# Optimization experiments

Measured on AMD Instinct MI355X. Metric: run time of the kernel, lower is better.

## Reference

```python
import jax, jax.numpy as jnp
import numpy as np

B, N, D, P, HMUL, K = 2, 4096, 64, 64, 4, 16
H = D * HMUL  # attn_mlp hidden = 256
EPS = 1e-5


def setup_inputs() -> dict:
    key = jax.random.key(0)
    ks = jax.random.split(key, 18)
    def lin(k, fan_in, shape):
        return (jax.random.normal(k, shape, dtype=jnp.float32) / np.sqrt(fan_in)).astype(jnp.float32)
    return {
        "x": jax.random.normal(ks[0], (B, N, D), dtype=jnp.float32),
        "pos": jax.random.uniform(ks[1], (B, N, 3), dtype=jnp.float32),
        "w_qkv": lin(ks[2], D, (D, 3 * D)), "b_qkv": jnp.zeros((3 * D,), jnp.float32),
        "w_p1": lin(ks[3], 3, (3, P)),     "b_p1": jnp.zeros((P,), jnp.float32),
        "w_p2": lin(ks[4], P, (P, D)),     "b_p2": jnp.zeros((D,), jnp.float32),
        "w_a1": lin(ks[5], D, (D, H)),     "b_a1": jnp.zeros((H,), jnp.float32),
        "w_a2": lin(ks[6], H, (H, D)),     "b_a2": jnp.zeros((D,), jnp.float32),
        "w_fc": lin(ks[7], D, (D, D)),     "b_fc": jnp.zeros((D,), jnp.float32),
        "gamma": jnp.ones((D,), jnp.float32), "beta": jnp.zeros((D,), jnp.float32),
    }


def reference(x, pos, w_qkv, b_qkv, w_p1, b_p1, w_p2, b_p2,
              w_a1, b_a1, w_a2, b_a2, w_fc, b_fc, gamma, beta):
    residual = x
    qkv = x @ w_qkv + b_qkv                      # [B,N,3D]
    q, k, v = jnp.split(qkv, 3, axis=-1)         # each [B,N,D]

    # full O(N^2) pairwise distances for KNN (smallest-k)
    rel = pos[:, :, None, :] - pos[:, None, :, :]       # [B,N,N,3]
    dist = jnp.sqrt(jnp.sum(rel * rel, axis=-1))        # [B,N,N]
    _, idx = jax.lax.top_k(-dist, K)                    # [B,N,K] nearest indices

    # gather neighbors (gather commutes with the pointwise MLPs the torch
    # code applies before its neighbor_select, so math is identical)
    gather = jax.vmap(lambda arr, i: arr[i])            # arr:[N,*], i:[N,K] -> [N,K,*]
    k_nb = gather(k, idx)                               # [B,N,K,D]
    v_nb = gather(v, idx)                               # [B,N,K,D]
    pos_nb = gather(pos, idx)                           # [B,N,K,3]

    qk_map = q[:, :, None, :] - k_nb                    # [B,N,K,D]
    rel_nb = pos[:, :, None, :] - pos_nb                # [B,N,K,3]
    pos_emb = jax.nn.relu(rel_nb @ w_p1 + b_p1) @ w_p2 + b_p2   # [B,N,K,D]

    h = qk_map + pos_emb
    scores = jax.nn.relu(h @ w_a1 + b_a1) @ w_a2 + b_a2          # [B,N,K,D]
    attn = jax.nn.softmax(scores, axis=-2)                       # over K neighbors
    agg = jnp.sum(attn * v_nb, axis=-2)                          # [B,N,D]

    agg = agg @ w_fc + b_fc
    # BatchNorm1d over channel dim D (training-mode batch stats over B and N)
    mean = jnp.mean(agg, axis=(0, 1))
    var = jnp.mean(jnp.square(agg - mean), axis=(0, 1))
    agg = (agg - mean) * jax.lax.rsqrt(var + EPS) * gamma + beta
    return jax.nn.relu(agg) + residual
```

## Files before the change

kernel.cpp:

```cpp
#include <hip/hip_runtime.h>
#include <hip/hip_bf16.h>
#include <math.h>

#define NPTS 4096
#define KNB 16
#define CAP 384
#define QPB 8

typedef __attribute__((ext_vector_type(8))) short bf16x8;
typedef __attribute__((ext_vector_type(4))) float f32x4;
#define MFMA16(a, b, c) __builtin_amdgcn_mfma_f32_16x16x32_bf16(a, b, c, 0, 0, 0)

__device__ __forceinline__ unsigned short f2bf(float f) {
  unsigned int u = __float_as_uint(f);
  unsigned int r = (u + 0x7fffu + ((u >> 16) & 1u)) >> 16;
  return (unsigned short)r;
}

__global__ __launch_bounds__(256) void qkv_pack_kernel(
    const float* __restrict__ x, const float* __restrict__ w_qkv,
    const float* __restrict__ b_qkv, float* __restrict__ qkv,
    const float* __restrict__ w_a1, const float* __restrict__ w_a2,
    const float* __restrict__ w_p2, unsigned short* __restrict__ pk1,
    unsigned short* __restrict__ pk2, unsigned short* __restrict__ pkp,
    float* __restrict__ stats) {
  int tid = threadIdx.x, bid = blockIdx.x;

  if (bid == 272) {
    if (tid < 128) stats[tid] = 0.f;
    return;
  }
  if (bid >= 128) {
    int e = (bid - 128) * 256 + tid;
    if (e < 16384) {
      int j = e & 7, lane = (e >> 3) & 63, t = e >> 9;
      int ks = t & 1, nt = t >> 1;
      int k = ks * 32 + ((lane >> 4) << 3) + j, n = nt * 16 + (lane & 15);
      pk1[e] = f2bf(w_a1[k * 256 + n]);
    } else if (e < 32768) {
      int e2 = e - 16384;
      int j = e2 & 7, lane = (e2 >> 3) & 63, t = e2 >> 9;
      int ks = t & 7, nt = t >> 3;
      int k = ks * 32 + ((lane >> 4) << 3) + j, n = nt * 16 + (lane & 15);
      pk2[e2] = f2bf(w_a2[k * 64 + n]);
    } else if (e < 36864) {
      int e3 = e - 32768;
      int j = e3 & 7, lane = (e3 >> 3) & 63, t = e3 >> 9;
      int ks = t & 1, nt = t >> 1;
      int k = ks * 32 + ((lane >> 4) << 3) + j, n = nt * 16 + (lane & 15);
      pkp[e3] = f2bf(w_p2[k * 64 + n]);
    }
    return;
  }

  int lane = tid & 63, w = tid >> 6;
  int m = lane & 15, quad = lane >> 4;
  int r0w = bid * 64 + w * 16;

  const float* xr = x + (size_t)(r0w + m) * 64;
  float xa[8], xb[8];
  *(float4*)&xa[0] = *(const float4*)(xr + quad * 8);
  *(float4*)&xa[4] = *(const float4*)(xr + quad * 8 + 4);
  *(float4*)&xb[0] = *(const float4*)(xr + 32 + quad * 8);
  *(float4*)&xb[4] = *(const float4*)(xr + 32 + quad * 8 + 4);
  bf16x8 a0, a1;
#pragma unroll
  for (int j = 0; j < 8; ++j) {
    a0[j] = (short)f2bf(xa[j]);
    a1[j] = (short)f2bf(xb[j]);
  }

#pragma unroll 4
  for (int nt = 0; nt < 12; ++nt) {
    int n = nt * 16 + m;
    int k0 = quad * 8;
    bf16x8 b0, b1;
#pragma unroll
    for (int j = 0; j < 8; ++j) {
      b0[j] = (short)f2bf(w_qkv[(size_t)(k0 + j) * 192 + n]);
      b1[j] = (short)f2bf(w_qkv[(size_t)(32 + k0 + j) * 192 + n]);
    }
    f32x4 acc = {0.f, 0.f, 0.f, 0.f};
    acc = MFMA16(a0, b0, acc);
    acc = MFMA16(a1, b1, acc);
    float bb = b_qkv[n];
#pragma unroll
    for (int i = 0; i < 4; ++i)
      qkv[(size_t)(r0w + quad * 4 + i) * 192 + n] = acc[i] + bb;
  }
}

__global__ __launch_bounds__(256, 4) void fused_kernel(
    const float* __restrict__ qkv, const float* __restrict__ pos,
    const unsigned short* __restrict__ pk1,
    const unsigned short* __restrict__ pk2,
    const unsigned short* __restrict__ pkp, const float* __restrict__ w_p1,
    const float* __restrict__ b_p1, const float* __restrict__ b_p2,
    const float* __restrict__ b_a1, const float* __restrict__ b_a2,
    const float* __restrict__ w_fc, const float* __restrict__ b_fc,
    float* __restrict__ y, float* __restrict__ stats) {
  __shared__ __align__(16) char smem[25216];
  __shared__ int s_idx[128];

  int tid = threadIdx.x, lane = tid & 63, w = tid >> 6;
  int m = lane & 15, quad = lane >> 4;
  int g0 = blockIdx.x * QPB;
  int b = g0 >> 12;
  const float* posb = pos + (size_t)b * NPTS * 3;

  {
    unsigned int(*cbits)[CAP] = (unsigned int(*)[CAP])smem;
    int(*cidx)[CAP] = (int(*)[CAP])(smem + 12288);
    unsigned long long* wmin = (unsigned long long*)(smem + 24576);
    float* sretry = (float*)(smem + 24608);
    unsigned int* scnt = (unsigned int*)(smem + 24640);
    unsigned long long* sprev = (unsigned long long*)(smem + 24672);
    int* sany = (int*)(smem + 24680);

    float qx[QPB], qy[QPB], qz[QPB];
#pragma unroll
    for (int q = 0; q < QPB; ++q) {
      int i = (g0 + q) & (NPTS - 1);
      qx[q] = posb[i * 3 + 0];
      qy[q] = posb[i * 3 + 1];
      qz[q] = posb[i * 3 + 2];
    }
    if (tid < QPB) scnt[tid] = 0;
    if (tid == 0) sany[0] = 0;
    __syncthreads();

    const float T2 = 0.015625f;
    for (int c = 0; c < NPTS / 256; ++c) {
      int j = c * 256 + tid;
      int j3 = j * 3;
      float px = posb[j3 + 0], py = posb[j3 + 1], pz = posb[j3 + 2];
#pragma unroll
      for (int q = 0; q < QPB; ++q) {
        float dx = qx[q] - px, dy = qy[q] - py, dz = qz[q] - pz;
        float d2 = fmaf(dz, dz, fmaf(dy, dy, dx * dx));
        bool hit = d2 < T2;
        unsigned long long mask = __ballot(hit);
        if (mask) {
          if (hit) {
            unsigned int p = atomicAdd(&scnt[q], 1u);
            if (p < CAP) {
              cbits[q][p] = __float_as_uint(d2);
              cidx[q][p] = j;
            }
          }
        }
      }
    }
    __syncthreads();

    if (tid < QPB) {
      int q = tid;
      unsigned int n = scnt[q];
      float nt = 0.f;
      if (n < KNB) nt = 0.0625f;
      else if (n > CAP) nt = 0.00390625f;
      sretry[q] = nt;
      if (nt != 0.f) {
        scnt[q] = 0;
        sany[0] = 1;
      }
    }
    __syncthreads();

    if (sany[0]) {
      float tr[QPB];
#pragma unroll
      for (int q = 0; q < QPB; ++q) tr[q] = sretry[q];
      for (int c = 0; c < NPTS / 256; ++c) {
        int j = c * 256 + tid;
        int j3 = j * 3;
        float px = posb[j3 + 0], py = posb[j3 + 1], pz = posb[j3 + 2];
#pragma unroll
        for (int q = 0; q < QPB; ++q) {
          if (tr[q] != 0.f) {
            float dx = qx[q] - px, dy = qy[q] - py, dz = qz[q] - pz;
            float d2 = fmaf(dz, dz, fmaf(dy, dy, dx * dx));
            bool hit = d2 < tr[q];
            unsigned long long mask = __ballot(hit);
            if (mask) {
              if (hit) {
                unsigned int p = atomicAdd(&scnt[q], 1u);
                if (p < CAP) {
                  cbits[q][p] = __float_as_uint(d2);
                  cidx[q][p] = j;
                }
              }
            }
          }
        }
      }
      __syncthreads();
    }

    for (int qq = 0; qq < 2; ++qq) {
      int q = w * 2 + qq;
      int L = (int)scnt[q];
      if (L >= KNB && L <= CAP) {
        for (int i = lane; i < L; i += 64) {
          unsigned long long ki = ((unsigned long long)cbits[q][i] << 32) |
                                  (unsigned int)cidx[q][i];
          int rank = 0;
          for (int mm = 0; mm < L; ++mm) {
            unsigned long long km = ((unsigned long long)cbits[q][mm] << 32) |
                                    (unsigned int)cidx[q][mm];
            rank += km < ki;
          }
          if (rank < KNB) s_idx[q * KNB + rank] = cidx[q][i];
        }
      }
    }
    __syncthreads();

    for (int q = 0; q < QPB; ++q) {
      unsigned int n = scnt[q];
      if (n < KNB || n > CAP) {
        unsigned long long prev = 0ull;
        for (int r = 0; r < KNB; ++r) {
          unsigned long long best = ~0ull;
          for (int c = 0; c < NPTS / 256; ++c) {
            int j = c * 256 + tid;
            float dx = qx[q] - posb[j * 3 + 0];
            float dy = qy[q] - posb[j * 3 + 1];
            float dz = qz[q] - posb[j * 3 + 2];
            float d2 = fmaf(dz, dz, fmaf(dy, dy, dx * dx));
            unsigned long long key =
                ((unsigned long long)__float_as_uint(d2) << 32) |
                (unsigned int)j;
            bool ok = (r == 0) || (key > prev);
            best = (ok && key < best) ? key : best;
          }
#pragma unroll
          for (int off = 32; off > 0; off >>= 1) {
            unsigned long long o = __shfl_down(best, off);
            best = best < o ? best : o;
          }
          if (lane == 0) wmin[w] = best;
          __syncthreads();
          if (tid == 0) {
            unsigned long long m0 = wmin[0], m1 = wmin[1];
            unsigned long long m2 = wmin[2], m3 = wmin[3];
            unsigned long long a = m0 < m1 ? m0 : m1;
            unsigned long long d = m2 < m3 ? m2 : m3;
            a = a < d ? a : d;
            s_idx[q * KNB + r] = (int)(unsigned int)a;
            sprev[0] = a;
          }
          __syncthreads();
          prev = sprev[0];
          __syncthreads();
        }
      }
    }
  }
  __syncthreads();

  unsigned short(*region)[72] = (unsigned short(*)[72])smem;
  float(*s_rel)[32][3] = (float(*)[32][3])(smem + 18432);

  if (lane < 32) {
    int row = 32 * w + lane;
    int p = lane >> 4;
    int g = g0 + 2 * w + p;
    int jb = (b << 12) | s_idx[row];
    s_rel[w][lane][0] = pos[(size_t)g * 3 + 0] - pos[(size_t)jb * 3 + 0];
    s_rel[w][lane][1] = pos[(size_t)g * 3 + 1] - pos[(size_t)jb * 3 + 1];
    s_rel[w][lane][2] = pos[(size_t)g * 3 + 2] - pos[(size_t)jb * 3 + 2];
  }

  {
    float w0 = w_p1[lane], w1 = w_p1[64 + lane], w2 = w_p1[128 + lane];
    float bp = b_p1[lane];
    for (int rl = 0; rl < 32; ++rl) {
      int row = 32 * w + rl;
      float rx = s_rel[w][rl][0], ry = s_rel[w][rl][1], rz = s_rel[w][rl][2];
      float e = fmaf(rz, w2, fmaf(ry, w1, fmaf(rx, w0, bp)));
      region[row][lane] = f2bf(fmaxf(e, 0.f));
    }
  }

  {
    bf16x8 ea0[2], ea1[2];
#pragma unroll
    for (int p = 0; p < 2; ++p) {
      ea0[p] = *(const bf16x8*)&region[32 * w + 16 * p + m][quad * 8];
      ea1[p] = *(const bf16x8*)&region[32 * w + 16 * p + m][32 + quad * 8];
    }
#pragma unroll
    for (int nt = 0; nt < 4; ++nt) {
      bf16x8 b0 = *(const bf16x8*)(pkp + ((size_t)(nt * 2 + 0) * 64 + lane) * 8);
      bf16x8 b1 = *(const bf16x8*)(pkp + ((size_t)(nt * 2 + 1) * 64 + lane) * 8);
      int col = nt * 16 + m;
      float bp2 = b_p2[col];
#pragma unroll
      for (int p = 0; p < 2; ++p) {
        f32x4 acc = {0.f, 0.f, 0.f, 0.f};
        acc = MFMA16(ea0[p], b0, acc);
        acc = MFMA16(ea1[p], b1, acc);
        int g = g0 + 2 * w + p;
        float qv = qkv[(size_t)g * 192 + col];
#pragma unroll
        for (int i = 0; i < 4; ++i) {
          int row = 32 * w + 16 * p + quad * 4 + i;
          int jb = (b << 12) | s_idx[row];
          float kv = qkv[(size_t)jb * 192 + 64 + col];
          region[row][col] = f2bf(qv - kv + acc[i] + bp2);
        }
      }
    }
  }

  float vreg[2][4][4];
#pragma unroll
  for (int p = 0; p < 2; ++p)
#pragma unroll
    for (int i = 0; i < 4; ++i) {
      int row = 32 * w + 16 * p + quad * 4 + i;
      int jb = (b << 12) | s_idx[row];
      const float* vr = qkv + (size_t)jb * 192 + 128;
#pragma unroll
      for (int nt2 = 0; nt2 < 4; ++nt2) vreg[p][nt2][i] = vr[nt2 * 16 + m];
    }

  bf16x8 ha0[2], ha1[2];
#pragma unroll
  for (int p = 0; p < 2; ++p) {
    ha0[p] = *(const bf16x8*)&region[32 * w + 16 * p + m][quad * 8];
    ha1[p] = *(const bf16x8*)&region[32 * w + 16 * p + m][32 + quad * 8];
  }
  f32x4 acc2[2][4];
#pragma unroll
  for (int p = 0; p < 2; ++p)
#pragma unroll
    for (int nt2 = 0; nt2 < 4; ++nt2) acc2[p][nt2] = (f32x4){0.f, 0.f, 0.f, 0.f};

  unsigned short(*s_tc)[72] = (unsigned short(*)[72])(smem + w * 4608);

#pragma unroll
  for (int c = 0; c < 4; ++c) {
#pragma unroll
    for (int ntc = 0; ntc < 4; ++ntc) {
      int nt = 4 * c + ntc;
      bf16x8 b0 = *(const bf16x8*)(pk1 + ((size_t)(nt * 2 + 0) * 64 + lane) * 8);
      bf16x8 b1 = *(const bf16x8*)(pk1 + ((size_t)(nt * 2 + 1) * 64 + lane) * 8);
      int coll = ntc * 16 + m;
      float ba = b_a1[nt * 16 + m];
#pragma unroll
      for (int p = 0; p < 2; ++p) {
        f32x4 t = {0.f, 0.f, 0.f, 0.f};
        t = MFMA16(ha0[p], b0, t);
        t = MFMA16(ha1[p], b1, t);
#pragma unroll
        for (int i = 0; i < 4; ++i)
          s_tc[16 * p + quad * 4 + i][coll] = f2bf(fmaxf(t[i] + ba, 0.f));
      }
    }
#pragma unroll
    for (int sub = 0; sub < 2; ++sub) {
      int ks = c * 2 + sub;
      bf16x8 a[2];
#pragma unroll
      for (int p = 0; p < 2; ++p)
        a[p] = *(const bf16x8*)&s_tc[16 * p + m][sub * 32 + quad * 8];
#pragma unroll
      for (int nt2 = 0; nt2 < 4; ++nt2) {
        bf16x8 bb =
            *(const bf16x8*)(pk2 + ((size_t)(nt2 * 8 + ks) * 64 + lane) * 8);
#pragma unroll
        for (int p = 0; p < 2; ++p) acc2[p][nt2] = MFMA16(a[p], bb, acc2[p][nt2]);
      }
    }
  }

  float ba2[4];
#pragma unroll
  for (int nt2 = 0; nt2 < 4; ++nt2) ba2[nt2] = b_a2[nt2 * 16 + m];
  float aggv[2][4];
#pragma unroll
  for (int p = 0; p < 2; ++p) {
#pragma unroll
    for (int nt2 = 0; nt2 < 4; ++nt2) {
      float sc[4];
#pragma unroll
      for (int i = 0; i < 4; ++i) sc[i] = acc2[p][nt2][i] + ba2[nt2];
      float mx = fmaxf(fmaxf(sc[0], sc[1]), fmaxf(sc[2], sc[3]));
      mx = fmaxf(mx, __shfl_xor(mx, 16));
      mx = fmaxf(mx, __shfl_xor(mx, 32));
      float ex[4], ss = 0.f;
#pragma unroll
      for (int i = 0; i < 4; ++i) {
        ex[i] = exp2f((sc[i] - mx) * 1.4426950408889634f);
        ss += ex[i];
      }
      ss += __shfl_xor(ss, 16);
      ss += __shfl_xor(ss, 32);
      float nu = 0.f;
#pragma unroll
      for (int i = 0; i < 4; ++i) nu = fmaf(ex[i], vreg[p][nt2][i], nu);
      nu += __shfl_xor(nu, 16);
      nu += __shfl_xor(nu, 32);
      aggv[p][nt2] = nu / ss;
    }
  }
  __syncthreads();

  float* s_agg = (float*)smem;
  if (quad == 0) {
#pragma unroll
    for (int p = 0; p < 2; ++p)
#pragma unroll
      for (int nt2 = 0; nt2 < 4; ++nt2)
        s_agg[(2 * w + p) * 64 + nt2 * 16 + m] = aggv[p][nt2];
  }
  __syncthreads();

  {
    int c = lane, r = w;
    float acc0 = b_fc[c], acc1 = b_fc[c];
    for (int d = 0; d < 64; ++d) {
      float wv = w_fc[d * 64 + c];
      acc0 = fmaf(s_agg[r * 64 + d], wv, acc0);
      acc1 = fmaf(s_agg[(r + 4) * 64 + d], wv, acc1);
    }
    y[(size_t)(g0 + r) * 64 + c] = acc0;
    y[(size_t)(g0 + r + 4) * 64 + c] = acc1;
    float* s_red = (float*)(smem + 2048);
    float* s_red2 = (float*)(smem + 3072);
    s_red[w * 64 + c] = acc0 + acc1;
    s_red2[w * 64 + c] = acc0 * acc0 + acc1 * acc1;
  }
  __syncthreads();
  if (tid < 64) {
    float* s_red = (float*)(smem + 2048);
    float* s_red2 = (float*)(smem + 3072);
    float s = s_red[tid] + s_red[64 + tid] + s_red[128 + tid] + s_red[192 + tid];
    float s2 =
        s_red2[tid] + s_red2[64 + tid] + s_red2[128 + tid] + s_red2[192 + tid];
    atomicAdd(&stats[tid], s);
    atomicAdd(&stats[64 + tid], s2);
  }
}

__global__ __launch_bounds__(256) void bn_kernel(
    const float* __restrict__ y, const float* __restrict__ x,
    const float* __restrict__ stats, const float* __restrict__ gamma,
    const float* __restrict__ beta, float* __restrict__ out) {
  size_t o = (size_t)blockIdx.x * 256 + threadIdx.x;
  int c = (int)(o & 63);
  const float inv_n = 1.f / 8192.f;
  float mean = stats[c] * inv_n;
  float var = stats[64 + c] * inv_n - mean * mean;
  float inv = rsqrtf(var + 1e-5f);
  float v = (y[o] - mean) * inv * gamma[c] + beta[c];
  out[o] = fmaxf(v, 0.f) + x[o];
}

extern "C" void kernel_launch(void* const* d_in, const int* in_sizes, int n_in,
                              void* d_out, int out_size, void* d_ws,
                              size_t ws_size, hipStream_t stream) {
  const float* x = (const float*)d_in[0];
  const float* pos = (const float*)d_in[1];
  const float* w_qkv = (const float*)d_in[2];
  const float* b_qkv = (const float*)d_in[3];
  const float* w_p1 = (const float*)d_in[4];
  const float* b_p1 = (const float*)d_in[5];
  const float* w_p2 = (const float*)d_in[6];
  const float* b_p2 = (const float*)d_in[7];
  const float* w_a1 = (const float*)d_in[8];
  const float* b_a1 = (const float*)d_in[9];
  const float* w_a2 = (const float*)d_in[10];
  const float* b_a2 = (const float*)d_in[11];
  const float* w_fc = (const float*)d_in[12];
  const float* b_fc = (const float*)d_in[13];
  const float* gamma = (const float*)d_in[14];
  const float* beta = (const float*)d_in[15];

  char* ws = (char*)d_ws;
  float* qkv = (float*)(ws + 0);
  float* y = (float*)(ws + 8912896);
  float* stats = (float*)(ws + 11010048);
  unsigned short* pk1 = (unsigned short*)(ws + 11010560);
  unsigned short* pk2 = (unsigned short*)(ws + 11043328);
  unsigned short* pkp = (unsigned short*)(ws + 11076096);

  hipLaunchKernelGGL(qkv_pack_kernel, dim3(273), dim3(256), 0, stream, x,
                     w_qkv, b_qkv, qkv, w_a1, w_a2, w_p2, pk1, pk2, pkp,
                     stats);
  hipLaunchKernelGGL(fused_kernel, dim3(1024), dim3(256), 0, stream, qkv, pos,
                     pk1, pk2, pkp, w_p1, b_p1, b_p2, b_a1, b_a2, w_fc, b_fc,
                     y, stats);
  hipLaunchKernelGGL(bn_kernel, dim3(2048), dim3(256), 0, stream, y, x, stats,
                     gamma, beta, (float*)d_out);
}
```

Baseline: 151.9 us.

## Halve queries per block and use a density-adaptive per-query KNN radius

Each block of the fused kernel now handles 4 query points instead of 8. Per-block shared memory drops, the candidate cap is halved, the launch-bounds occupancy hint is raised and the grid is doubled. The fixed KNN search radius is replaced with a per-query radius estimated from uniform point density with boundary clipping, aiming for about 48 candidates, and retry thresholds now scale from that radius. The aim is higher occupancy and fewer retry passes for queries near the box edges. The cost is that every block rescans all 4096 positions for fewer queries, and the radius estimate assumes a roughly uniform point cloud, falling back to retries otherwise.

```diff
diff --git a/kernel.cpp b/kernel.cpp
--- a/kernel.cpp
+++ b/kernel.cpp
@@ -4,8 +4,8 @@
 
 #define NPTS 4096
 #define KNB 16
-#define CAP 384
-#define QPB 8
+#define CAP 192
+#define QPB 4
 
 typedef __attribute__((ext_vector_type(8))) short bf16x8;
 typedef __attribute__((ext_vector_type(4))) float f32x4;
@@ -90,7 +90,7 @@
   }
 }
 
-__global__ __launch_bounds__(256, 4) void fused_kernel(
+__global__ __launch_bounds__(256, 8) void fused_kernel(
     const float* __restrict__ qkv, const float* __restrict__ pos,
     const unsigned short* __restrict__ pk1,
     const unsigned short* __restrict__ pk2,
@@ -99,8 +99,8 @@
     const float* __restrict__ b_a1, const float* __restrict__ b_a2,
     const float* __restrict__ w_fc, const float* __restrict__ b_fc,
     float* __restrict__ y, float* __restrict__ stats) {
-  __shared__ __align__(16) char smem[25216];
-  __shared__ int s_idx[128];
+  __shared__ __align__(16) char smem[9984];
+  __shared__ int s_idx[64];
 
   int tid = threadIdx.x, lane = tid & 63, w = tid >> 6;
   int m = lane & 15, quad = lane >> 4;
@@ -110,14 +110,14 @@
 
   {
     unsigned int(*cbits)[CAP] = (unsigned int(*)[CAP])smem;
-    int(*cidx)[CAP] = (int(*)[CAP])(smem + 12288);
-    unsigned long long* wmin = (unsigned long long*)(smem + 24576);
-    float* sretry = (float*)(smem + 24608);
-    unsigned int* scnt = (unsigned int*)(smem + 24640);
-    unsigned long long* sprev = (unsigned long long*)(smem + 24672);
-    int* sany = (int*)(smem + 24680);
-
-    float qx[QPB], qy[QPB], qz[QPB];
+    int(*cidx)[CAP] = (int(*)[CAP])(smem + 3072);
+    unsigned long long* wmin = (unsigned long long*)(smem + 6144);
+    float* sretry = (float*)(smem + 6176);
+    unsigned int* scnt = (unsigned int*)(smem + 6192);
+    unsigned long long* sprev = (unsigned long long*)(smem + 6208);
+    int* sany = (int*)(smem + 6216);
+
+    float qx[QPB], qy[QPB], qz[QPB], t2q[QPB];
 #pragma unroll
     for (int q = 0; q < QPB; ++q) {
       int i = (g0 + q) & (NPTS - 1);
@@ -125,11 +125,26 @@
       qy[q] = posb[i * 3 + 1];
       qz[q] = posb[i * 3 + 2];
     }
+#pragma unroll
+    for (int q = 0; q < QPB; ++q) {
+      float r = 0.141f;
+#pragma unroll
+      for (int it = 0; it < 3; ++it) {
+        float inv2r = 0.5f / r;
+        float fx = (fminf(qx[q] + r, 1.f) - fmaxf(qx[q] - r, 0.f)) * inv2r;
+        float fy = (fminf(qy[q] + r, 1.f) - fmaxf(qy[q] - r, 0.f)) * inv2r;
+        float fz = (fminf(qz[q] + r, 1.f) - fmaxf(qz[q] - r, 0.f)) * inv2r;
+        float expn = 17157.28f * r * r * r * fx * fy * fz;
+        float s = exp2f(0.33333334f * log2f(48.f / expn));
+        s = fminf(fmaxf(s, 0.7f), 1.6f);
+        r = fminf(r * s, 0.32f);
+      }
+      t2q[q] = r * r;
+    }
     if (tid < QPB) scnt[tid] = 0;
     if (tid == 0) sany[0] = 0;
     __syncthreads();
 
-    const float T2 = 0.015625f;
     for (int c = 0; c < NPTS / 256; ++c) {
       int j = c * 256 + tid;
       int j3 = j * 3;
@@ -138,7 +153,7 @@
       for (int q = 0; q < QPB; ++q) {
         float dx = qx[q] - px, dy = qy[q] - py, dz = qz[q] - pz;
         float d2 = fmaf(dz, dz, fmaf(dy, dy, dx * dx));
-        bool hit = d2 < T2;
+        bool hit = d2 < t2q[q];
         unsigned long long mask = __ballot(hit);
         if (mask) {
           if (hit) {
@@ -157,8 +172,8 @@
       int q = tid;
       unsigned int n = scnt[q];
       float nt = 0.f;
-      if (n < KNB) nt = 0.0625f;
-      else if (n > CAP) nt = 0.00390625f;
+      if (n < KNB) nt = t2q[q] * 4.f;
+      else if (n > CAP) nt = t2q[q] * 0.4f;
       sretry[q] = nt;
       if (nt != 0.f) {
         scnt[q] = 0;
@@ -197,8 +212,8 @@
       __syncthreads();
     }
 
-    for (int qq = 0; qq < 2; ++qq) {
-      int q = w * 2 + qq;
+    {
+      int q = w;
       int L = (int)scnt[q];
       if (L >= KNB && L <= CAP) {
         for (int i = lane; i < L; i += 64) {
@@ -260,12 +275,11 @@
   __syncthreads();
 
   unsigned short(*region)[72] = (unsigned short(*)[72])smem;
-  float(*s_rel)[32][3] = (float(*)[32][3])(smem + 18432);
-
-  if (lane < 32) {
-    int row = 32 * w + lane;
-    int p = lane >> 4;
-    int g = g0 + 2 * w + p;
+  float(*s_rel)[16][3] = (float(*)[16][3])(smem + 9216);
+
+  if (lane < 16) {
+    int row = 16 * w + lane;
+    int g = g0 + w;
     int jb = (b << 12) | s_idx[row];
     s_rel[w][lane][0] = pos[(size_t)g * 3 + 0] - pos[(size_t)jb * 3 + 0];
     s_rel[w][lane][1] = pos[(size_t)g * 3 + 1] - pos[(size_t)jb * 3 + 1];
@@ -275,8 +289,8 @@
   {
     float w0 = w_p1[lane], w1 = w_p1[64 + lane], w2 = w_p1[128 + lane];
     float bp = b_p1[lane];
-    for (int rl = 0; rl < 32; ++rl) {
-      int row = 32 * w + rl;
+    for (int rl = 0; rl < 16; ++rl) {
+      int row = 16 * w + rl;
       float rx = s_rel[w][rl][0], ry = s_rel[w][rl][1], rz = s_rel[w][rl][2];
       float e = fmaf(rz, w2, fmaf(ry, w1, fmaf(rx, w0, bp)));
       region[row][lane] = f2bf(fmaxf(e, 0.f));
@@ -284,61 +298,46 @@
   }
 
   {
-    bf16x8 ea0[2], ea1[2];
-#pragma unroll
-    for (int p = 0; p < 2; ++p) {
-      ea0[p] = *(const bf16x8*)&region[32 * w + 16 * p + m][quad * 8];
-      ea1[p] = *(const bf16x8*)&region[32 * w + 16 * p + m][32 + quad * 8];
-    }
+    bf16x8 ea0 = *(const bf16x8*)&region[16 * w + m][quad * 8];
+    bf16x8 ea1 = *(const bf16x8*)&region[16 * w + m][32 + quad * 8];
+    int g = g0 + w;
 #pragma unroll
     for (int nt = 0; nt < 4; ++nt) {
       bf16x8 b0 = *(const bf16x8*)(pkp + ((size_t)(nt * 2 + 0) * 64 + lane) * 8);
       bf16x8 b1 = *(const bf16x8*)(pkp + ((size_t)(nt * 2 + 1) * 64 + lane) * 8);
       int col = nt * 16 + m;
       float bp2 = b_p2[col];
-#pragma unroll
-      for (int p = 0; p < 2; ++p) {
-        f32x4 acc = {0.f, 0.f, 0.f, 0.f};
-        acc = MFMA16(ea0[p], b0, acc);
-        acc = MFMA16(ea1[p], b1, acc);
-        int g = g0 + 2 * w + p;
-        float qv = qkv[(size_t)g * 192 + col];
-#pragma unroll
-        for (int i = 0; i < 4; ++i) {
-          int row = 32 * w + 16 * p + quad * 4 + i;
-          int jb = (b << 12) | s_idx[row];
-          float kv = qkv[(size_t)jb * 192 + 64 + col];
-          region[row][col] = f2bf(qv - kv + acc[i] + bp2);
-        }
-      }
-    }
-  }
-
-  float vreg[2][4][4];
-#pragma unroll
-  for (int p = 0; p < 2; ++p)
-#pragma unroll
-    for (int i = 0; i < 4; ++i) {
-      int row = 32 * w + 16 * p + quad * 4 + i;
-      int jb = (b << 12) | s_idx[row];
-      const float* vr = qkv + (size_t)jb * 192 + 128;
-#pragma unroll
-      for (int nt2 = 0; nt2 < 4; ++nt2) vreg[p][nt2][i] = vr[nt2 * 16 + m];
-    }
-
-  bf16x8 ha0[2], ha1[2];
-#pragma unroll
-  for (int p = 0; p < 2; ++p) {
-    ha0[p] = *(const bf16x8*)&region[32 * w + 16 * p + m][quad * 8];
-    ha1[p] = *(const bf16x8*)&region[32 * w + 16 * p + m][32 + quad * 8];
-  }
-  f32x4 acc2[2][4];
-#pragma unroll
-  for (int p = 0; p < 2; ++p)
-#pragma unroll
-    for (int nt2 = 0; nt2 < 4; ++nt2) acc2[p][nt2] = (f32x4){0.f, 0.f, 0.f, 0.f};
-
-  unsigned short(*s_tc)[72] = (unsigned short(*)[72])(smem + w * 4608);
+      f32x4 acc = {0.f, 0.f, 0.f, 0.f};
+      acc = MFMA16(ea0, b0, acc);
+      acc = MFMA16(ea1, b1, acc);
+      float qv = qkv[(size_t)g * 192 + col];
+#pragma unroll
+      for (int i = 0; i < 4; ++i) {
+        int row = 16 * w + quad * 4 + i;
+        int jb = (b << 12) | s_idx[row];
+        float kv = qkv[(size_t)jb * 192 + 64 + col];
+        region[row][col] = f2bf(qv - kv + acc[i] + bp2);
+      }
+    }
+  }
+
+  float vreg[4][4];
+#pragma unroll
+  for (int i = 0; i < 4; ++i) {
+    int row = 16 * w + quad * 4 + i;
+    int jb = (b << 12) | s_idx[row];
+    const float* vr = qkv + (size_t)jb * 192 + 128;
+#pragma unroll
+    for (int nt2 = 0; nt2 < 4; ++nt2) vreg[nt2][i] = vr[nt2 * 16 + m];
+  }
+
+  bf16x8 ha0 = *(const bf16x8*)&region[16 * w + m][quad * 8];
+  bf16x8 ha1 = *(const bf16x8*)&region[16 * w + m][32 + quad * 8];
+  f32x4 acc2[4];
+#pragma unroll
+  for (int nt2 = 0; nt2 < 4; ++nt2) acc2[nt2] = (f32x4){0.f, 0.f, 0.f, 0.f};
+
+  unsigned short(*s_tc)[72] = (unsigned short(*)[72])(smem + w * 2304);
 
 #pragma unroll
   for (int c = 0; c < 4; ++c) {
@@ -349,29 +348,22 @@
       bf16x8 b1 = *(const bf16x8*)(pk1 + ((size_t)(nt * 2 + 1) * 64 + lane) * 8);
       int coll = ntc * 16 + m;
       float ba = b_a1[nt * 16 + m];
-#pragma unroll
-      for (int p = 0; p < 2; ++p) {
-        f32x4 t = {0.f, 0.f, 0.f, 0.f};
-        t = MFMA16(ha0[p], b0, t);
-        t = MFMA16(ha1[p], b1, t);
-#pragma unroll
-        for (int i = 0; i < 4; ++i)
-          s_tc[16 * p + quad * 4 + i][coll] = f2bf(fmaxf(t[i] + ba, 0.f));
-      }
+      f32x4 t = {0.f, 0.f, 0.f, 0.f};
+      t = MFMA16(ha0, b0, t);
+      t = MFMA16(ha1, b1, t);
+#pragma unroll
+      for (int i = 0; i < 4; ++i)
+        s_tc[quad * 4 + i][coll] = f2bf(fmaxf(t[i] + ba, 0.f));
     }
 #pragma unroll
     for (int sub = 0; sub < 2; ++sub) {
       int ks = c * 2 + sub;
-      bf16x8 a[2];
-#pragma unroll
-      for (int p = 0; p < 2; ++p)
-        a[p] = *(const bf16x8*)&s_tc[16 * p + m][sub * 32 + quad * 8];
+      bf16x8 a = *(const bf16x8*)&s_tc[m][sub * 32 + quad * 8];
 #pragma unroll
       for (int nt2 = 0; nt2 < 4; ++nt2) {
         bf16x8 bb =
             *(const bf16x8*)(pk2 + ((size_t)(nt2 * 8 + ks) * 64 + lane) * 8);
-#pragma unroll
-        for (int p = 0; p < 2; ++p) acc2[p][nt2] = MFMA16(a[p], bb, acc2[p][nt2]);
+        acc2[nt2] = MFMA16(a, bb, acc2[nt2]);
       }
     }
   }
@@ -379,64 +371,55 @@
   float ba2[4];
 #pragma unroll
   for (int nt2 = 0; nt2 < 4; ++nt2) ba2[nt2] = b_a2[nt2 * 16 + m];
-  float aggv[2][4];
-#pragma unroll
-  for (int p = 0; p < 2; ++p) {
-#pragma unroll
-    for (int nt2 = 0; nt2 < 4; ++nt2) {
-      float sc[4];
-#pragma unroll
-      for (int i = 0; i < 4; ++i) sc[i] = acc2[p][nt2][i] + ba2[nt2];
-      float mx = fmaxf(fmaxf(sc[0], sc[1]), fmaxf(sc[2], sc[3]));
-      mx = fmaxf(mx, __shfl_xor(mx, 16));
-      mx = fmaxf(mx, __shfl_xor(mx, 32));
-      float ex[4], ss = 0.f;
-#pragma unroll
-      for (int i = 0; i < 4; ++i) {
-        ex[i] = exp2f((sc[i] - mx) * 1.4426950408889634f);
-        ss += ex[i];
-      }
-      ss += __shfl_xor(ss, 16);
-      ss += __shfl_xor(ss, 32);
-      float nu = 0.f;
-#pragma unroll
-      for (int i = 0; i < 4; ++i) nu = fmaf(ex[i], vreg[p][nt2][i], nu);
-      nu += __shfl_xor(nu, 16);
-      nu += __shfl_xor(nu, 32);
-      aggv[p][nt2] = nu / ss;
-    }
+  float aggv[4];
+#pragma unroll
+  for (int nt2 = 0; nt2 < 4; ++nt2) {
+    float sc[4];
+#pragma unroll
+    for (int i = 0; i < 4; ++i) sc[i] = acc2[nt2][i] + ba2[nt2];
+    float mx = fmaxf(fmaxf(sc[0], sc[1]), fmaxf(sc[2], sc[3]));
+    mx = fmaxf(mx, __shfl_xor(mx, 16));
+    mx = fmaxf(mx, __shfl_xor(mx, 32));
+    float ex[4], ss = 0.f;
+#pragma unroll
+    for (int i = 0; i < 4; ++i) {
+      ex[i] = exp2f((sc[i] - mx) * 1.4426950408889634f);
+      ss += ex[i];
+    }
+    ss += __shfl_xor(ss, 16);
+    ss += __shfl_xor(ss, 32);
+    float nu = 0.f;
+#pragma unroll
+    for (int i = 0; i < 4; ++i) nu = fmaf(ex[i], vreg[nt2][i], nu);
+    nu += __shfl_xor(nu, 16);
+    nu += __shfl_xor(nu, 32);
+    aggv[nt2] = nu / ss;
   }
   __syncthreads();
 
   float* s_agg = (float*)smem;
   if (quad == 0) {
 #pragma unroll
-    for (int p = 0; p < 2; ++p)
-#pragma unroll
-      for (int nt2 = 0; nt2 < 4; ++nt2)
-        s_agg[(2 * w + p) * 64 + nt2 * 16 + m] = aggv[p][nt2];
+    for (int nt2 = 0; nt2 < 4; ++nt2)
+      s_agg[w * 64 + nt2 * 16 + m] = aggv[nt2];
   }
   __syncthreads();
 
   {
     int c = lane, r = w;
-    float acc0 = b_fc[c], acc1 = b_fc[c];
-    for (int d = 0; d < 64; ++d) {
-      float wv = w_fc[d * 64 + c];
-      acc0 = fmaf(s_agg[r * 64 + d], wv, acc0);
-      acc1 = fmaf(s_agg[(r + 4) * 64 + d], wv, acc1);
-    }
+    float acc0 = b_fc[c];
+    for (int d = 0; d < 64; ++d)
+      acc0 = fmaf(s_agg[r * 64 + d], w_fc[d * 64 + c], acc0);
     y[(size_t)(g0 + r) * 64 + c] = acc0;
-    y[(size_t)(g0 + r + 4) * 64 + c] = acc1;
-    float* s_red = (float*)(smem + 2048);
-    float* s_red2 = (float*)(smem + 3072);
-    s_red[w * 64 + c] = acc0 + acc1;
-    s_red2[w * 64 + c] = acc0 * acc0 + acc1 * acc1;
+    float* s_red = (float*)(smem + 1024);
+    float* s_red2 = (float*)(smem + 2048);
+    s_red[w * 64 + c] = acc0;
+    s_red2[w * 64 + c] = acc0 * acc0;
   }
   __syncthreads();
   if (tid < 64) {
-    float* s_red = (float*)(smem + 2048);
-    float* s_red2 = (float*)(smem + 3072);
+    float* s_red = (float*)(smem + 1024);
+    float* s_red2 = (float*)(smem + 2048);
     float s = s_red[tid] + s_red[64 + tid] + s_red[128 + tid] + s_red[192 + tid];
     float s2 =
         s_red2[tid] + s_red2[64 + tid] + s_red2[128 + tid] + s_red2[192 + tid];
@@ -490,7 +473,7 @@
   hipLaunchKernelGGL(qkv_pack_kernel, dim3(273), dim3(256), 0, stream, x,
                      w_qkv, b_qkv, qkv, w_a1, w_a2, w_p2, pk1, pk2, pkp,
                      stats);
-  hipLaunchKernelGGL(fused_kernel, dim3(1024), dim3(256), 0, stream, qkv, pos,
+  hipLaunchKernelGGL(fused_kernel, dim3(2048), dim3(256), 0, stream, qkv, pos,
                      pk1, pk2, pkp, w_p1, b_p1, b_p2, b_a1, b_a2, w_fc, b_fc,
                      y, stats);
   hipLaunchKernelGGL(bn_kernel, dim3(2048), dim3(256), 0, stream, y, x, stats,
```

After: 188.9 us. 1.24x slower.
